# Performance work log

Hardware: AMD Instinct MI355X
Metric: run time of the kernel (lower is better)

## Reference

```python
import jax, jax.numpy as jnp
import numpy as np

D = 256      # embedding_dim
DI = 512     # inner dim = proj_factor * D
H = 4        # num heads
DH = DI // H # head dim
L = 4        # num blocks
K = 4        # causal conv kernel size

def _ln(x, g, b):
    mu = jnp.mean(x, -1, keepdims=True)
    v = jnp.var(x, -1, keepdims=True)
    return (x - mu) * jax.lax.rsqrt(v + 1e-5) * g + b

def _causal_conv(x, w, b):
    # x [B,S,DI], w [K,DI] depthwise causal conv
    S = x.shape[1]
    xp = jnp.pad(x, ((0, 0), (K - 1, 0), (0, 0)))
    out = b
    for j in range(K):
        out = out + xp[:, j:j + S, :] * w[j]
    return out

def _mlstm(q, k, v, ip, fp):
    # parallel stabilized mLSTM. q,k,v [B,S,H,DH]; ip,fp [B,S,H]
    q = q.transpose(0, 2, 1, 3)
    k = k.transpose(0, 2, 1, 3)
    v = v.transpose(0, 2, 1, 3)
    ip = ip.transpose(0, 2, 1)  # [B,H,S]
    fp = fp.transpose(0, 2, 1)
    lf = jax.nn.log_sigmoid(fp)                      # log forget gates
    Fc = jnp.cumsum(lf, axis=-1)
    Fc = jnp.concatenate([jnp.zeros_like(Fc[..., :1]), Fc], axis=-1)  # [B,H,S+1]
    logfg = Fc[..., 1:, None] - Fc[..., None, 1:]    # [B,H,S,S]: sum of log f over (s,t]
    S_len = q.shape[2]
    tri = jnp.tril(jnp.ones((S_len, S_len), dtype=bool))
    logD = jnp.where(tri, logfg + ip[..., None, :], jnp.float32(-1e30))
    m = jnp.max(logD, axis=-1, keepdims=True)        # stabilizer
    Dm = jnp.exp(logD - m)
    qk = jnp.einsum('bhtd,bhsd->bhts', q, k) * (DH ** -0.5)
    C = qk * Dm
    norm = jnp.maximum(jnp.abs(jnp.sum(C, axis=-1, keepdims=True)), jnp.exp(-m))
    h = jnp.einsum('bhts,bhsd->bhtd', C / (norm + 1e-6), v)
    return h.transpose(0, 2, 1, 3)

def _forward(x, time_features, Wp, bp, ln_g, ln_b, Wup, bup, conv_w, conv_b,
             Wq, Wk, Wv, Wif, bif, gn_g, gn_b, skip, Wdown, bdown,
             lnf_g, lnf_b, Wf, bf):
    B, S = x.shape
    xi = jnp.concatenate([x[..., None], time_features], axis=-1)  # [B,S,5]
    h = xi @ Wp + bp                                              # [B,S,D]
    for l in range(L):
        res = h
        hn = _ln(h, ln_g[l], ln_b[l])
        up = hn @ Wup[l] + bup[l]                 # [B,S,2*DI]
        xm, z = up[..., :DI], up[..., DI:]
        xc = jax.nn.silu(_causal_conv(xm, conv_w[l], conv_b[l]))
        q = (xc @ Wq[l]).reshape(B, S, H, DH)
        k = (xc @ Wk[l]).reshape(B, S, H, DH)
        v = (xm @ Wv[l]).reshape(B, S, H, DH)
        gi = jnp.concatenate([q.reshape(B, S, DI), k.reshape(B, S, DI), v.reshape(B, S, DI)], axis=-1)
        gates = gi @ Wif[l] + bif[l]              # [B,S,2H]
        ht = _mlstm(q, k, v, gates[..., :H], gates[..., H:])  # [B,S,H,DH]
        ht = _ln(ht, gn_g[l].reshape(H, DH), gn_b[l].reshape(H, DH)).reshape(B, S, DI)
        ht = ht + skip[l] * xc
        ht = ht * jax.nn.silu(z)
        h = res + ht @ Wdown[l] + bdown[l]
    h = _ln(h, lnf_g, lnf_b)
    return h[:, -1, :] @ Wf + bf                  # [B,1]

def setup_inputs():
    key = jax.random.key(0)
    ks = jax.random.split(key, 16)
    B, S = 8, 1024
    sd = jnp.float32(0.02)
    return {
        'x': jax.random.normal(ks[0], (B, S), jnp.float32),
        'time_features': jax.random.normal(ks[1], (B, S, 4), jnp.float32),
        'Wp': jax.random.normal(ks[2], (5, D)) * sd, 'bp': jnp.zeros((D,)),
        'ln_g': jnp.ones((L, D)), 'ln_b': jnp.zeros((L, D)),
        'Wup': jax.random.normal(ks[3], (L, D, 2 * DI)) * sd, 'bup': jnp.zeros((L, 2 * DI)),
        'conv_w': jax.random.normal(ks[4], (L, K, DI)) * sd, 'conv_b': jnp.zeros((L, DI)),
        'Wq': jax.random.normal(ks[5], (L, DI, DI)) * sd,
        'Wk': jax.random.normal(ks[6], (L, DI, DI)) * sd,
        'Wv': jax.random.normal(ks[7], (L, DI, DI)) * sd,
        'Wif': jax.random.normal(ks[8], (L, 3 * DI, 2 * H)) * sd, 'bif': jnp.zeros((L, 2 * H)),
        'gn_g': jnp.ones((L, DI)), 'gn_b': jnp.zeros((L, DI)),
        'skip': jnp.ones((L, DI)),
        'Wdown': jax.random.normal(ks[9], (L, DI, D)) * sd, 'bdown': jnp.zeros((L, D)),
        'lnf_g': jnp.ones((D,)), 'lnf_b': jnp.zeros((D,)),
        'Wf': jax.random.normal(ks[10], (D, 1)) * sd, 'bf': jnp.zeros((1,)),
    }

def reference(x, time_features, Wp, bp, ln_g, ln_b, Wup, bup, conv_w, conv_b,
              Wq, Wk, Wv, Wif, bif, gn_g, gn_b, skip, Wdown, bdown,
              lnf_g, lnf_b, Wf, bf):
    return _forward(x, time_features, Wp, bp, ln_g, ln_b, Wup, bup, conv_w, conv_b,
                    Wq, Wk, Wv, Wif, bif, gn_g, gn_b, skip, Wdown, bdown,
                    lnf_g, lnf_b, Wf, bf)
```

## Files before the change

### kernel.cpp

```cpp
#include <hip/hip_runtime.h>
#include <hip/hip_bf16.h>
#include <math.h>

#define S 1024
#define NLAYER 4

typedef __bf16 bf16x8 __attribute__((ext_vector_type(8)));
typedef float floatx4 __attribute__((ext_vector_type(4)));

__device__ __forceinline__ float wave_sum(float v) {
  #pragma unroll
  for (int off = 32; off > 0; off >>= 1) v += __shfl_xor(v, off, 64);
  return v;
}

__device__ __forceinline__ void wtrans_body(
    int bid, const float* Wup, const float* Wq, const float* Wk, const float* Wv,
    const float* Wdown, __bf16* WupT, __bf16* WqkT, __bf16* WvT, __bf16* WdownT) {
  __shared__ float T[32][33];
  int layer = bid / 1152, rr = bid % 1152;
  const float* src; __bf16* dst; int K, N, tile;
  if (rr < 256)       { src = Wup   + layer * 262144; dst = WupT  + layer * 262144;          K = 256; N = 1024; tile = rr; }
  else if (rr < 512)  { src = Wq    + layer * 262144; dst = WqkT  + layer * 524288;          K = 512; N = 512;  tile = rr - 256; }
  else if (rr < 768)  { src = Wk    + layer * 262144; dst = WqkT  + layer * 524288 + 262144; K = 512; N = 512;  tile = rr - 512; }
  else if (rr < 1024) { src = Wv    + layer * 262144; dst = WvT   + layer * 262144;          K = 512; N = 512;  tile = rr - 768; }
  else                { src = Wdown + layer * 131072; dst = WdownT + layer * 131072;         K = 512; N = 256;  tile = rr - 1024; }
  int ntn = N >> 5;
  int tk = tile / ntn, tn = tile % ntn;
  int tid = threadIdx.x;
  int r = tid >> 3, c4 = (tid & 7) * 4;
  float4 v = *(const float4*)(src + (size_t)(tk * 32 + r) * N + tn * 32 + c4);
  T[c4 + 0][r] = v.x; T[c4 + 1][r] = v.y; T[c4 + 2][r] = v.z; T[c4 + 3][r] = v.w;
  __syncthreads();
  __bf16 o[4];
  #pragma unroll
  for (int j = 0; j < 4; ++j) o[j] = (__bf16)T[r][c4 + j];
  *(uint2*)(dst + (size_t)(tn * 32 + r) * K + tk * 32 + c4) = *(uint2*)o;
}

__device__ __forceinline__ void wgprep_body(
    int bid, const float* Wq, const float* Wk, const float* Wv,
    const float* Wif, float* wg) {
  int l = bid >> 8;
  int rem = bid & 255;
  int sel = rem >> 7;
  int kg = rem & 127;
  int tid = threadIdx.x;
  int wv = tid >> 6, lane = tid & 63;
  int k = kg * 4 + wv;
  const float* wif = Wif + (size_t)l * 1536 * 8;
  float part[8] = {0, 0, 0, 0, 0, 0, 0, 0};
  if (sel == 0) {
    const float* qr = Wq + (size_t)l * 262144 + (size_t)k * 512;
    const float* kr = Wk + (size_t)l * 262144 + (size_t)k * 512;
    #pragma unroll
    for (int i = 0; i < 8; ++i) {
      int n = lane + i * 64;
      float qv = qr[n], kv = kr[n];
      const float* wq8 = wif + (size_t)n * 8;
      const float* wk8 = wif + (size_t)(512 + n) * 8;
      #pragma unroll
      for (int j = 0; j < 8; ++j) part[j] += qv * wq8[j] + kv * wk8[j];
    }
  } else {
    const float* vr = Wv + (size_t)l * 262144 + (size_t)k * 512;
    #pragma unroll
    for (int i = 0; i < 8; ++i) {
      int n = lane + i * 64;
      float vv = vr[n];
      const float* wv8 = wif + (size_t)(1024 + n) * 8;
      #pragma unroll
      for (int j = 0; j < 8; ++j) part[j] += vv * wv8[j];
    }
  }
  #pragma unroll
  for (int j = 0; j < 8; ++j) part[j] = wave_sum(part[j]);
  if (lane < 8) wg[(size_t)l * 8192 + sel * 4096 + (size_t)k * 8 + lane] = part[lane];
}

__device__ __forceinline__ void embed_body(
    int row, const float* x, const float* tf, const float* Wp, const float* bp,
    const float* g, const float* b, float* h, __bf16* hn) {
  int n = threadIdx.x;
  float xv = x[row];
  const float* t4 = tf + (size_t)row * 4;
  float acc = bp[n] + xv * Wp[n];
  acc += t4[0] * Wp[256 + n];
  acc += t4[1] * Wp[512 + n];
  acc += t4[2] * Wp[768 + n];
  acc += t4[3] * Wp[1024 + n];
  h[(size_t)row * 256 + n] = acc;
  __shared__ float red[4];
  int wid = n >> 6, lane = n & 63;
  float s = wave_sum(acc);
  if (lane == 0) red[wid] = s;
  __syncthreads();
  float mu = (red[0] + red[1] + red[2] + red[3]) * (1.f / 256.f);
  __syncthreads();
  float d = acc - mu;
  float s2 = wave_sum(d * d);
  if (lane == 0) red[wid] = s2;
  __syncthreads();
  float var = (red[0] + red[1] + red[2] + red[3]) * (1.f / 256.f);
  float rs = rsqrtf(var + 1e-5f);
  hn[(size_t)row * 256 + n] = (__bf16)(d * rs * g[n] + b[n]);
}

__global__ __launch_bounds__(256) void prep_kernel(
    const float* __restrict__ x, const float* __restrict__ tf,
    const float* __restrict__ Wp, const float* __restrict__ bp,
    const float* __restrict__ ln_g, const float* __restrict__ ln_b,
    const float* __restrict__ Wup, const float* __restrict__ Wq,
    const float* __restrict__ Wk, const float* __restrict__ Wv,
    const float* __restrict__ Wdown, const float* __restrict__ Wif,
    __bf16* __restrict__ WupT, __bf16* __restrict__ WqkT,
    __bf16* __restrict__ WvT, __bf16* __restrict__ WdownT,
    float* __restrict__ wg, float* __restrict__ h, __bf16* __restrict__ hn) {
  int bid = blockIdx.x;
  if (bid < 4608) {
    wtrans_body(bid, Wup, Wq, Wk, Wv, Wdown, WupT, WqkT, WvT, WdownT);
  } else if (bid < 4608 + 1024) {
    wgprep_body(bid - 4608, Wq, Wk, Wv, Wif, wg);
  } else {
    embed_body(bid - 5632, x, tf, Wp, bp, ln_g, ln_b, h, hn);
  }
}

template <int TM, int MODE, int ACC>
__device__ __forceinline__ void hgemm_body(
    char* smem_raw,
    const __bf16* __restrict__ A, int lda,
    const __bf16* __restrict__ BT, int Kdim,
    const float* __restrict__ bias,
    void* __restrict__ Cout, int ldc, int bxi, int byi) {
  auto As = (__bf16(*)[40])smem_raw;
  auto Bs = (__bf16(*)[40])(smem_raw + (size_t)TM * 160);
  int tid = threadIdx.x;
  int bm = bxi * TM, bn = byi * 128;
  int wid = tid >> 6, lane = tid & 63;
  int wr = wid >> 1, wc = wid & 1;
  int lg = lane >> 4, li = lane & 15;
  constexpr int MI = TM / 32;
  constexpr int WROW = TM / 2;
  floatx4 acc[MI][4];
  #pragma unroll
  for (int i = 0; i < MI; ++i)
    #pragma unroll
    for (int j = 0; j < 4; ++j) acc[i][j] = (floatx4)(0.f);

  int arow = tid >> 2, aseg = tid & 3;
  bf16x8 pa0, pa1, pb0, pb1;
  auto pre = [&](int k0) {
    pa0 = *(const bf16x8*)(A + (size_t)(bm + arow) * lda + k0 + aseg * 8);
    if constexpr (TM == 128)
      pa1 = *(const bf16x8*)(A + (size_t)(bm + arow + 64) * lda + k0 + aseg * 8);
    pb0 = *(const bf16x8*)(BT + (size_t)(bn + arow) * Kdim + k0 + aseg * 8);
    pb1 = *(const bf16x8*)(BT + (size_t)(bn + arow + 64) * Kdim + k0 + aseg * 8);
  };
  auto stor = [&](int buf) {
    *(bf16x8*)&As[buf * TM + arow][aseg * 8] = pa0;
    if constexpr (TM == 128) *(bf16x8*)&As[buf * TM + arow + 64][aseg * 8] = pa1;
    *(bf16x8*)&Bs[buf * 128 + arow][aseg * 8] = pb0;
    *(bf16x8*)&Bs[buf * 128 + arow + 64][aseg * 8] = pb1;
  };
  pre(0);
  stor(0);
  if (32 < Kdim) pre(32);
  int cur = 0;
  for (int k0 = 0; k0 < Kdim; k0 += 32) {
    __syncthreads();
    bf16x8 af[MI], bfr[4];
    #pragma unroll
    for (int mi = 0; mi < MI; ++mi)
      af[mi] = *(const bf16x8*)&As[cur * TM + wr * WROW + mi * 16 + li][lg * 8];
    #pragma unroll
    for (int ni = 0; ni < 4; ++ni)
      bfr[ni] = *(const bf16x8*)&Bs[cur * 128 + wc * 64 + ni * 16 + li][lg * 8];
    #pragma unroll
    for (int mi = 0; mi < MI; ++mi)
      #pragma unroll
      for (int ni = 0; ni < 4; ++ni)
        acc[mi][ni] = __builtin_amdgcn_mfma_f32_16x16x32_bf16(af[mi], bfr[ni], acc[mi][ni], 0, 0, 0);
    if (k0 + 32 < Kdim) {
      stor(cur ^ 1);
      if (k0 + 64 < Kdim) pre(k0 + 64);
    }
    cur ^= 1;
  }
  if constexpr (MODE == 1) {
    __bf16* eb = (__bf16*)smem_raw;
    const int PITCH = 136;
    __bf16* C = (__bf16*)Cout;
    #pragma unroll
    for (int mi = 0; mi < MI; ++mi) {
      __syncthreads();
      #pragma unroll
      for (int ni = 0; ni < 4; ++ni) {
        int col = wc * 64 + ni * 16 + li;
        float bz = bias ? bias[bn + col] : 0.f;
        #pragma unroll
        for (int r = 0; r < 4; ++r) {
          int lr = wr * 16 + lg * 4 + r;
          eb[lr * PITCH + col] = (__bf16)(acc[mi][ni][r] + bz);
        }
      }
      __syncthreads();
      #pragma unroll
      for (int i = 0; i < 2; ++i) {
        int lr = (tid >> 4) + i * 16;
        int c8 = (tid & 15) * 8;
        bf16x8 v = *(const bf16x8*)&eb[lr * PITCH + c8];
        int row_g = bm + (lr >> 4) * 64 + mi * 16 + (lr & 15);
        *(bf16x8*)(C + (size_t)row_g * ldc + bn + c8) = v;
      }
    }
  } else {
    #pragma unroll
    for (int mi = 0; mi < MI; ++mi) {
      int row = bm + wr * WROW + mi * 16 + lg * 4;
      #pragma unroll
      for (int ni = 0; ni < 4; ++ni) {
        int col = bn + wc * 64 + ni * 16 + li;
        if constexpr (MODE == 2) {
          __bf16 o4[4];
          #pragma unroll
          for (int r = 0; r < 4; ++r) o4[r] = (__bf16)acc[mi][ni][r];
          __bf16* vt = (__bf16*)Cout;
          size_t off = ((size_t)((row >> 10) * 4 + (col >> 7)) * 128 + (col & 127)) * 1024 + (row & 1023);
          *(uint2*)(vt + off) = *(uint2*)o4;
        } else {
          float bz = bias ? bias[col] : 0.f;
          float* C = (float*)Cout;
          #pragma unroll
          for (int r = 0; r < 4; ++r) {
            float v = acc[mi][ni][r] + bz;
            if (ACC) v += C[(size_t)(row + r) * ldc + col];
            C[(size_t)(row + r) * ldc + col] = v;
          }
        }
      }
    }
  }
}

template <int TM, int MODE, int ACC>
__global__ __launch_bounds__(256) void hgemm(
    const __bf16* __restrict__ A, int lda,
    const __bf16* __restrict__ BT, int Kdim,
    const float* __restrict__ bias,
    void* __restrict__ Cout, int ldc) {
  extern __shared__ char smem[];
  hgemm_body<TM, MODE, ACC>(smem, A, lda, BT, Kdim, bias, Cout, ldc,
                            blockIdx.x, blockIdx.y);
}

__device__ __forceinline__ void scan_body(
    int bh, int lane, const float* __restrict__ gates, float* __restrict__ gout,
    float* __restrict__ Mout, float* __restrict__ NFout) {
  int bb = bh >> 2, hh = bh & 3;
  float ip[16], pf[16];
  #pragma unroll
  for (int i = 0; i < 16; ++i) {
    int t = lane * 16 + i;
    const float* grow = gates + ((size_t)(bb * S + t)) * 8;
    ip[i] = grow[hh];
    float fp = grow[4 + hh];
    float lf = fminf(fp, 0.f) - log1pf(__expf(-fabsf(fp)));
    pf[i] = (i == 0) ? lf : pf[i - 1] + lf;
  }
  float T = pf[15];
  float inc = T;
  #pragma unroll
  for (int off = 1; off < 64; off <<= 1) {
    float v = __shfl_up(inc, off, 64);
    if (lane >= off) inc += v;
  }
  float excl = inc - T;
  float F[16], g[16], pm[16];
  #pragma unroll
  for (int i = 0; i < 16; ++i) {
    F[i] = excl + pf[i];
    g[i] = ip[i] - F[i];
    pm[i] = (i == 0) ? g[0] : fmaxf(pm[i - 1], g[i]);
  }
  float Mx = pm[15];
  float incm = Mx;
  #pragma unroll
  for (int off = 1; off < 64; off <<= 1) {
    float v = __shfl_up(incm, off, 64);
    if (lane >= off) incm = fmaxf(incm, v);
  }
  float em = __shfl_up(incm, 1, 64);
  if (lane == 0) em = -3.4e38f;
  #pragma unroll
  for (int i = 0; i < 16; ++i) {
    int t = lane * 16 + i;
    size_t o = (size_t)bh * S + t;
    float M = fmaxf(em, pm[i]);
    gout[o] = g[i];
    Mout[o] = M;
    NFout[o] = __expf(-F[i] - M);
  }
}

__global__ __launch_bounds__(256) void qkv_kernel(
    const __bf16* __restrict__ xc, const __bf16* __restrict__ WqkT,
    __bf16* __restrict__ qk, const __bf16* __restrict__ up,
    const __bf16* __restrict__ WvT, __bf16* __restrict__ vT,
    const float* __restrict__ gates, float* __restrict__ gbuf,
    float* __restrict__ Mbuf, float* __restrict__ NFbuf) {
  extern __shared__ char smem[];
  if (blockIdx.y < 8) {
    hgemm_body<128, 1, 0>(smem, xc, 512, WqkT, 512, nullptr, qk, 1024,
                          blockIdx.x, blockIdx.y);
  } else if (blockIdx.y < 16) {
    int j = blockIdx.y - 8;
    hgemm_body<64, 2, 0>(smem, up, 1024, WvT, 512, nullptr, vT, 0,
                         blockIdx.x * 2 + (j & 1), j >> 1);
  } else {
    if (blockIdx.x < 32 && threadIdx.x < 64)
      scan_body(blockIdx.x, threadIdx.x, gates, gbuf, Mbuf, NFbuf);
  }
}

__global__ __launch_bounds__(256) void dgemm_ln_kernel(
    const __bf16* __restrict__ A, const __bf16* __restrict__ BT,
    const float* __restrict__ bias, float* __restrict__ h,
    const float* __restrict__ lng, const float* __restrict__ lnb,
    __bf16* __restrict__ hn,
    const float* __restrict__ lnfg, const float* __restrict__ lnfb,
    const float* __restrict__ Wf, const float* __restrict__ bf,
    float* __restrict__ out) {
  __shared__ __bf16 As[2 * 32][40];
  __shared__ __bf16 Bs[2 * 256][40];
  __shared__ float redS[2][32], redQ[2][32];
  int tid = threadIdx.x;
  int bm = blockIdx.x * 32;
  int wid = tid >> 6, lane = tid & 63;
  int wr = wid >> 1, wc = wid & 1;
  int lg = lane >> 4, li = lane & 15;
  floatx4 acc[8];
  #pragma unroll
  for (int j = 0; j < 8; ++j) acc[j] = (floatx4)(0.f);

  int arow = tid >> 2, aseg = tid & 3;
  bf16x8 pa, pb[4];
  auto pre = [&](int k0) {
    if (tid < 128)
      pa = *(const bf16x8*)(A + (size_t)(bm + arow) * 512 + k0 + aseg * 8);
    #pragma unroll
    for (int i = 0; i < 4; ++i)
      pb[i] = *(const bf16x8*)(BT + (size_t)(arow + i * 64) * 512 + k0 + aseg * 8);
  };
  auto stor = [&](int buf) {
    if (tid < 128) *(bf16x8*)&As[buf * 32 + arow][aseg * 8] = pa;
    #pragma unroll
    for (int i = 0; i < 4; ++i)
      *(bf16x8*)&Bs[buf * 256 + arow + i * 64][aseg * 8] = pb[i];
  };
  pre(0);
  stor(0);
  pre(32);
  int cur = 0;
  for (int k0 = 0; k0 < 512; k0 += 32) {
    __syncthreads();
    bf16x8 af = *(const bf16x8*)&As[cur * 32 + wr * 16 + li][lg * 8];
    #pragma unroll
    for (int ni = 0; ni < 8; ++ni) {
      bf16x8 bfr = *(const bf16x8*)&Bs[cur * 256 + wc * 128 + ni * 16 + li][lg * 8];
      acc[ni] = __builtin_amdgcn_mfma_f32_16x16x32_bf16(af, bfr, acc[ni], 0, 0, 0);
    }
    if (k0 + 32 < 512) {
      stor(cur ^ 1);
      if (k0 + 64 < 512) pre(k0 + 64);
    }
    cur ^= 1;
  }
  #pragma unroll
  for (int r = 0; r < 4; ++r) {
    int lr = wr * 16 + lg * 4 + r;
    int row = bm + lr;
    float s1 = 0.f, s2 = 0.f;
    #pragma unroll
    for (int ni = 0; ni < 8; ++ni) {
      int col = wc * 128 + ni * 16 + li;
      float v = acc[ni][r] + bias[col] + h[(size_t)row * 256 + col];
      acc[ni][r] = v;
      h[(size_t)row * 256 + col] = v;
      s1 += v;
      s2 += v * v;
    }
    s1 += __shfl_xor(s1, 1, 64); s1 += __shfl_xor(s1, 2, 64);
    s1 += __shfl_xor(s1, 4, 64); s1 += __shfl_xor(s1, 8, 64);
    s2 += __shfl_xor(s2, 1, 64); s2 += __shfl_xor(s2, 2, 64);
    s2 += __shfl_xor(s2, 4, 64); s2 += __shfl_xor(s2, 8, 64);
    if (li == 0) { redS[wc][lr] = s1; redQ[wc][lr] = s2; }
  }
  __syncthreads();
  if (lng) {
    #pragma unroll
    for (int r = 0; r < 4; ++r) {
      int lr = wr * 16 + lg * 4 + r;
      int row = bm + lr;
      float s1 = redS[0][lr] + redS[1][lr];
      float s2 = redQ[0][lr] + redQ[1][lr];
      float mu = s1 * (1.f / 256.f);
      float var = s2 * (1.f / 256.f) - mu * mu;
      float rs = rsqrtf(var + 1e-5f);
      #pragma unroll
      for (int ni = 0; ni < 8; ++ni) {
        int col = wc * 128 + ni * 16 + li;
        hn[(size_t)row * 256 + col] = (__bf16)((acc[ni][r] - mu) * rs * lng[col] + lnb[col]);
      }
    }
  } else if ((bm & 1023) == 992) {
    if (wr == 1 && lg == 3) {
      float s1 = redS[0][31] + redS[1][31];
      float s2 = redQ[0][31] + redQ[1][31];
      float mu = s1 * (1.f / 256.f);
      float var = s2 * (1.f / 256.f) - mu * mu;
      float rs = rsqrtf(var + 1e-5f);
      float p = 0.f;
      #pragma unroll
      for (int ni = 0; ni < 8; ++ni) {
        int col = wc * 128 + ni * 16 + li;
        float ln = (acc[ni][3] - mu) * rs * lnfg[col] + lnfb[col];
        p += ln * Wf[col];
      }
      p += __shfl_xor(p, 1, 64); p += __shfl_xor(p, 2, 64);
      p += __shfl_xor(p, 4, 64); p += __shfl_xor(p, 8, 64);
      if (li == 0) redS[wc][0] = p;
    }
    __syncthreads();
    if (tid == 0) out[bm >> 10] = redS[0][0] + redS[1][0] + bf[0];
  }
}

__global__ __launch_bounds__(256) void conv_silu_kernel(
    const __bf16* __restrict__ up, const float* __restrict__ cw,
    const float* __restrict__ cb, const float* __restrict__ wg,
    const float* __restrict__ bif, __bf16* __restrict__ xc,
    float* __restrict__ gates) {
  int tid = threadIdx.x;
  int wv = tid >> 6, lane = tid & 63;
  int row = blockIdx.x * 4 + wv;
  int c8 = lane * 8;
  int t = row & (S - 1);
  float acc[8];
  *(float4*)&acc[0] = *(const float4*)(cb + c8);
  *(float4*)&acc[4] = *(const float4*)(cb + c8 + 4);
  float xm[8];
  #pragma unroll
  for (int j = 0; j < 4; ++j) {
    int tt = t - 3 + j;
    if (tt >= 0) {
      bf16x8 xv = *(const bf16x8*)(up + (size_t)(row - 3 + j) * 1024 + c8);
      float4 w0 = *(const float4*)(cw + j * 512 + c8);
      float4 w1 = *(const float4*)(cw + j * 512 + c8 + 4);
      acc[0] += w0.x * (float)xv[0]; acc[1] += w0.y * (float)xv[1];
      acc[2] += w0.z * (float)xv[2]; acc[3] += w0.w * (float)xv[3];
      acc[4] += w1.x * (float)xv[4]; acc[5] += w1.y * (float)xv[5];
      acc[6] += w1.z * (float)xv[6]; acc[7] += w1.w * (float)xv[7];
      if (j == 3) {
        #pragma unroll
        for (int m = 0; m < 8; ++m) xm[m] = (float)xv[m];
      }
    }
  }
  bf16x8 o;
  float xcs[8];
  #pragma unroll
  for (int m = 0; m < 8; ++m) {
    float sg = 1.f / (1.f + __expf(-acc[m]));
    xcs[m] = acc[m] * sg;
    o[m] = (__bf16)xcs[m];
  }
  *(bf16x8*)(xc + (size_t)row * 512 + c8) = o;
  const float* w1 = wg + (size_t)c8 * 8;
  const float* w2 = wg + 4096 + (size_t)c8 * 8;
  float part[8] = {0, 0, 0, 0, 0, 0, 0, 0};
  #pragma unroll
  for (int m = 0; m < 8; ++m) {
    const float* a = w1 + m * 8;
    const float* b = w2 + m * 8;
    #pragma unroll
    for (int j = 0; j < 8; ++j) part[j] += xcs[m] * a[j] + xm[m] * b[j];
  }
  #pragma unroll
  for (int j = 0; j < 8; ++j) part[j] = wave_sum(part[j]);
  if (lane < 8) gates[(size_t)row * 8 + lane] = part[lane] + bif[lane];
}

__global__ __launch_bounds__(512, 1) void attn_kernel(
    const __bf16* __restrict__ qk, const __bf16* __restrict__ vT,
    const float* __restrict__ gbuf, const float* __restrict__ Mbuf,
    const float* __restrict__ NFbuf,
    const float* __restrict__ gn_g, const float* __restrict__ gn_b,
    const float* __restrict__ skip,
    const __bf16* __restrict__ xc, const __bf16* __restrict__ up,
    __bf16* __restrict__ hd) {
  __shared__ __bf16 Ks[64][136];
  __shared__ __bf16 Vs[128][72];
  __shared__ __bf16 plds[8][16][72];
  __shared__ float gls[64];
  __shared__ float glds[128], blds[128], slds[128];
  int px = blockIdx.y, bh = blockIdx.x;
  int tqA = px, tqB = 15 - px;
  int bb = bh >> 2, hh = bh & 3;
  int tid = threadIdx.x;
  int wv = tid >> 6, lane = tid & 63;
  int sel = wv >> 2, wl = wv & 3;
  int lg = lane >> 4, li = lane & 15;
  int tq = (sel == 0) ? tqA : tqB;
  int tb = tq * 64 + wl * 16;
  const float scale = 0.08838834764831845f;

  if (tid < 128) {
    glds[tid] = gn_g[hh * 128 + tid];
    blds[tid] = gn_b[hh * 128 + tid];
    slds[tid] = skip[hh * 128 + tid];
  }

  bf16x8 aq[4];
  {
    const __bf16* qp = qk + ((size_t)(bb * S + tb + li)) * 1024 + hh * 128 + lg * 8;
    #pragma unroll
    for (int cd = 0; cd < 4; ++cd) aq[cd] = *(const bf16x8*)(qp + cd * 32);
  }
  float ml[4], nf[4];
  #pragma unroll
  for (int r = 0; r < 4; ++r) {
    ml[r] = Mbuf[(size_t)bh * S + tb + lg * 4 + r];
    nf[r] = NFbuf[(size_t)bh * S + tb + lg * 4 + r];
  }

  floatx4 oacc[8];
  #pragma unroll
  for (int df = 0; df < 8; ++df) oacc[df] = (floatx4)(0.f);
  float rs[4] = {0, 0, 0, 0};

  int krow = tid >> 3, kcol = tid & 7;
  bf16x8 kreg0, kreg1, vreg0, vreg1;
  float greg = 0.f;
  auto preload = [&](int st) {
    int s0 = st * 64;
    const __bf16* kp = qk + ((size_t)(bb * S + s0 + krow)) * 1024 + 512 + hh * 128;
    kreg0 = *(const bf16x8*)(kp + kcol * 8);
    kreg1 = *(const bf16x8*)(kp + 64 + kcol * 8);
    vreg0 = *(const bf16x8*)(vT + ((size_t)(bh * 128 + krow)) * 1024 + s0 + kcol * 8);
    vreg1 = *(const bf16x8*)(vT + ((size_t)(bh * 128 + 64 + krow)) * 1024 + s0 + kcol * 8);
    if (tid < 64) greg = gbuf[(size_t)bh * S + s0 + tid];
  };
  preload(0);

  for (int st = 0; st <= tqB; ++st) {
    __syncthreads();
    *(bf16x8*)&Ks[krow][kcol * 8] = kreg0;
    *(bf16x8*)&Ks[krow][64 + kcol * 8] = kreg1;
    *(bf16x8*)&Vs[krow][kcol * 8] = vreg0;
    *(bf16x8*)&Vs[64 + krow][kcol * 8] = vreg1;
    if (tid < 64) gls[tid] = greg;
    __syncthreads();
    if (st < tqB) preload(st + 1);

    if (st <= tq) {
      int s0 = st * 64;
      #pragma unroll
      for (int ns = 0; ns < 4; ++ns) {
        bf16x8 bk0 = *(const bf16x8*)&Ks[ns * 16 + li][lg * 8];
        bf16x8 bk1 = *(const bf16x8*)&Ks[ns * 16 + li][32 + lg * 8];
        bf16x8 bk2 = *(const bf16x8*)&Ks[ns * 16 + li][64 + lg * 8];
        bf16x8 bk3 = *(const bf16x8*)&Ks[ns * 16 + li][96 + lg * 8];
        int s = s0 + ns * 16 + li;
        float gv = gls[ns * 16 + li];
        floatx4 pa = (floatx4)(0.f);
        pa = __builtin_amdgcn_mfma_f32_16x16x32_bf16(aq[0], bk0, pa, 0, 0, 0);
        pa = __builtin_amdgcn_mfma_f32_16x16x32_bf16(aq[1], bk1, pa, 0, 0, 0);
        pa = __builtin_amdgcn_mfma_f32_16x16x32_bf16(aq[2], bk2, pa, 0, 0, 0);
        pa = __builtin_amdgcn_mfma_f32_16x16x32_bf16(aq[3], bk3, pa, 0, 0, 0);
        #pragma unroll
        for (int r = 0; r < 4; ++r) {
          int t = tb + lg * 4 + r;
          float val = pa[r] * scale * __expf(gv - ml[r]);
          float w = (s <= t) ? val : 0.f;
          rs[r] += w;
          plds[wv][lg * 4 + r][ns * 16 + li] = (__bf16)w;
        }
      }
      bf16x8 ap0 = *(const bf16x8*)&plds[wv][li][lg * 8];
      bf16x8 ap1 = *(const bf16x8*)&plds[wv][li][32 + lg * 8];
      #pragma unroll
      for (int df = 0; df < 8; ++df) {
        bf16x8 bv0 = *(const bf16x8*)&Vs[df * 16 + li][lg * 8];
        bf16x8 bv1 = *(const bf16x8*)&Vs[df * 16 + li][32 + lg * 8];
        oacc[df] = __builtin_amdgcn_mfma_f32_16x16x32_bf16(ap0, bv0, oacc[df], 0, 0, 0);
        oacc[df] = __builtin_amdgcn_mfma_f32_16x16x32_bf16(ap1, bv1, oacc[df], 0, 0, 0);
      }
    }
  }
  #pragma unroll
  for (int r = 0; r < 4; ++r) {
    float a = rs[r];
    a += __shfl_xor(a, 1, 64); a += __shfl_xor(a, 2, 64);
    a += __shfl_xor(a, 4, 64); a += __shfl_xor(a, 8, 64);
    rs[r] = a;
  }
  #pragma unroll
  for (int r = 0; r < 4; ++r) {
    float inv = 1.f / (fmaxf(fabsf(rs[r]), nf[r]) + 1e-6f);
    float v8[8], s1 = 0.f, s2 = 0.f;
    #pragma unroll
    for (int df = 0; df < 8; ++df) {
      float v = oacc[df][r] * inv;
      v8[df] = v;
      s1 += v;
      s2 += v * v;
    }
    s1 += __shfl_xor(s1, 1, 64); s1 += __shfl_xor(s1, 2, 64);
    s1 += __shfl_xor(s1, 4, 64); s1 += __shfl_xor(s1, 8, 64);
    s2 += __shfl_xor(s2, 1, 64); s2 += __shfl_xor(s2, 2, 64);
    s2 += __shfl_xor(s2, 4, 64); s2 += __shfl_xor(s2, 8, 64);
    float mu = s1 * (1.f / 128.f);
    float var = s2 * (1.f / 128.f) - mu * mu;
    float rq = rsqrtf(var + 1e-5f);
    int t = tb + lg * 4 + r;
    const __bf16* xr = xc + ((size_t)(bb * S + t)) * 512 + hh * 128 + li;
    const __bf16* zr = up + ((size_t)(bb * S + t)) * 1024 + 512 + hh * 128 + li;
    __bf16* od = hd + ((size_t)(bb * S + t)) * 512 + hh * 128 + li;
    #pragma unroll
    for (int df = 0; df < 8; ++df) {
      int c = df * 16 + li;
      float ln = (v8[df] - mu) * rq * glds[c] + blds[c];
      float val = ln + slds[c] * (float)xr[df * 16];
      float z = (float)zr[df * 16];
      float sg = 1.f / (1.f + __expf(-z));
      od[df * 16] = (__bf16)(val * (z * sg));
    }
  }
}

extern "C" void kernel_launch(void* const* d_in, const int* in_sizes, int n_in,
                              void* d_out, int out_size, void* d_ws, size_t ws_size,
                              hipStream_t stream) {
  const float* x      = (const float*)d_in[0];
  const float* tf     = (const float*)d_in[1];
  const float* Wp     = (const float*)d_in[2];
  const float* bp     = (const float*)d_in[3];
  const float* ln_g   = (const float*)d_in[4];
  const float* ln_b   = (const float*)d_in[5];
  const float* Wup    = (const float*)d_in[6];
  const float* bup    = (const float*)d_in[7];
  const float* conv_w = (const float*)d_in[8];
  const float* conv_b = (const float*)d_in[9];
  const float* Wq     = (const float*)d_in[10];
  const float* Wk     = (const float*)d_in[11];
  const float* Wv     = (const float*)d_in[12];
  const float* Wif    = (const float*)d_in[13];
  const float* bif    = (const float*)d_in[14];
  const float* gn_g   = (const float*)d_in[15];
  const float* gn_b   = (const float*)d_in[16];
  const float* skip   = (const float*)d_in[17];
  const float* Wdown  = (const float*)d_in[18];
  const float* bdown  = (const float*)d_in[19];
  const float* lnf_g  = (const float*)d_in[20];
  const float* lnf_b  = (const float*)d_in[21];
  const float* Wf     = (const float*)d_in[22];
  const float* bf     = (const float*)d_in[23];
  float* out = (float*)d_out;

  float* h     = (float*)d_ws;
  float* gates = h + 2097152;
  float* gbuf  = gates + 65536;
  float* Mbuf  = gbuf + 32768;
  float* NFbuf = Mbuf + 32768;
  float* wgbuf = NFbuf + 32768;
  __bf16* hn   = (__bf16*)(wgbuf + 32768);
  __bf16* up   = hn + 2097152;
  __bf16* xc   = up + 8388608;
  __bf16* qk   = xc + 4194304;
  __bf16* vT   = qk + 8388608;
  __bf16* hd   = vT + 4194304;
  __bf16* WupT   = hd + 4194304;
  __bf16* WqkT   = WupT + 1048576;
  __bf16* WvT    = WqkT + 2097152;
  __bf16* WdownT = WvT + 1048576;

  prep_kernel<<<13824, 256, 0, stream>>>(
      x, tf, Wp, bp, ln_g, ln_b, Wup, Wq, Wk, Wv, Wdown, Wif,
      WupT, WqkT, WvT, WdownT, wgbuf, h, hn);
  for (int l = 0; l < NLAYER; ++l) {
    hgemm<128, 1, 0><<<dim3(64, 8), 256, 40960, stream>>>(
        hn, 256, WupT + (size_t)l * 262144, 256, bup + l * 1024, up, 1024);
    conv_silu_kernel<<<2048, 256, 0, stream>>>(up, conv_w + l * 2048, conv_b + l * 512,
                                               wgbuf + l * 8192, bif + l * 8, xc, gates);
    qkv_kernel<<<dim3(64, 17), 256, 40960, stream>>>(
        xc, WqkT + (size_t)l * 524288, qk, up, WvT + (size_t)l * 262144, vT,
        gates, gbuf, Mbuf, NFbuf);
    attn_kernel<<<dim3(32, 8), 512, 0, stream>>>(
        qk, vT, gbuf, Mbuf, NFbuf, gn_g + l * 512, gn_b + l * 512, skip + l * 512,
        xc, up, hd);
    const float* lng = (l + 1 < NLAYER) ? (ln_g + (l + 1) * 256) : nullptr;
    const float* lnb = (l + 1 < NLAYER) ? (ln_b + (l + 1) * 256) : nullptr;
    dgemm_ln_kernel<<<256, 256, 0, stream>>>(
        hd, WdownT + (size_t)l * 131072, bdown + l * 256, h, lng, lnb, hn,
        lnf_g, lnf_b, Wf, bf, out);
  }
}
```

Measured before the change: 593.9 us.

## Split paired-query-tile attention blocks into one 256-thread block per query tile

After: 588.8 us. About the same (-0.9%).

```diff
diff --git a/kernel.cpp b/kernel.cpp
--- a/kernel.cpp
+++ b/kernel.cpp
@@ -491,7 +491,7 @@
   if (lane < 8) gates[(size_t)row * 8 + lane] = part[lane] + bif[lane];
 }
 
-__global__ __launch_bounds__(512, 1) void attn_kernel(
+__global__ __launch_bounds__(256, 1) void attn_kernel(
     const __bf16* __restrict__ qk, const __bf16* __restrict__ vT,
     const float* __restrict__ gbuf, const float* __restrict__ Mbuf,
     const float* __restrict__ NFbuf,
@@ -501,18 +501,16 @@
     __bf16* __restrict__ hd) {
   __shared__ __bf16 Ks[64][136];
   __shared__ __bf16 Vs[128][72];
-  __shared__ __bf16 plds[8][16][72];
+  __shared__ __bf16 plds[4][16][72];
   __shared__ float gls[64];
   __shared__ float glds[128], blds[128], slds[128];
-  int px = blockIdx.y, bh = blockIdx.x;
-  int tqA = px, tqB = 15 - px;
+  int bh = blockIdx.x;
+  int tq = 15 - blockIdx.y;
   int bb = bh >> 2, hh = bh & 3;
   int tid = threadIdx.x;
   int wv = tid >> 6, lane = tid & 63;
-  int sel = wv >> 2, wl = wv & 3;
   int lg = lane >> 4, li = lane & 15;
-  int tq = (sel == 0) ? tqA : tqB;
-  int tb = tq * 64 + wl * 16;
+  int tb = tq * 64 + wv * 16;
   const float scale = 0.08838834764831845f;
 
   if (tid < 128) {
@@ -540,62 +538,65 @@
   float rs[4] = {0, 0, 0, 0};
 
   int krow = tid >> 3, kcol = tid & 7;
-  bf16x8 kreg0, kreg1, vreg0, vreg1;
+  bf16x8 kreg[4], vreg[4];
   float greg = 0.f;
   auto preload = [&](int st) {
     int s0 = st * 64;
     const __bf16* kp = qk + ((size_t)(bb * S + s0 + krow)) * 1024 + 512 + hh * 128;
-    kreg0 = *(const bf16x8*)(kp + kcol * 8);
-    kreg1 = *(const bf16x8*)(kp + 64 + kcol * 8);
-    vreg0 = *(const bf16x8*)(vT + ((size_t)(bh * 128 + krow)) * 1024 + s0 + kcol * 8);
-    vreg1 = *(const bf16x8*)(vT + ((size_t)(bh * 128 + 64 + krow)) * 1024 + s0 + kcol * 8);
+    kreg[0] = *(const bf16x8*)(kp + kcol * 8);
+    kreg[1] = *(const bf16x8*)(kp + (size_t)32 * 1024 + kcol * 8);
+    kreg[2] = *(const bf16x8*)(kp + 64 + kcol * 8);
+    kreg[3] = *(const bf16x8*)(kp + (size_t)32 * 1024 + 64 + kcol * 8);
+    #pragma unroll
+    for (int i = 0; i < 4; ++i)
+      vreg[i] = *(const bf16x8*)(vT + ((size_t)(bh * 128 + krow + i * 32)) * 1024 + s0 + kcol * 8);
     if (tid < 64) greg = gbuf[(size_t)bh * S + s0 + tid];
   };
   preload(0);
 
-  for (int st = 0; st <= tqB; ++st) {
+  for (int st = 0; st <= tq; ++st) {
     __syncthreads();
-    *(bf16x8*)&Ks[krow][kcol * 8] = kreg0;
-    *(bf16x8*)&Ks[krow][64 + kcol * 8] = kreg1;
-    *(bf16x8*)&Vs[krow][kcol * 8] = vreg0;
-    *(bf16x8*)&Vs[64 + krow][kcol * 8] = vreg1;
+    *(bf16x8*)&Ks[krow][kcol * 8] = kreg[0];
+    *(bf16x8*)&Ks[krow + 32][kcol * 8] = kreg[1];
+    *(bf16x8*)&Ks[krow][64 + kcol * 8] = kreg[2];
+    *(bf16x8*)&Ks[krow + 32][64 + kcol * 8] = kreg[3];
+    #pragma unroll
+    for (int i = 0; i < 4; ++i) *(bf16x8*)&Vs[krow + i * 32][kcol * 8] = vreg[i];
     if (tid < 64) gls[tid] = greg;
     __syncthreads();
-    if (st < tqB) preload(st + 1);
-
-    if (st <= tq) {
-      int s0 = st * 64;
-      #pragma unroll
-      for (int ns = 0; ns < 4; ++ns) {
-        bf16x8 bk0 = *(const bf16x8*)&Ks[ns * 16 + li][lg * 8];
-        bf16x8 bk1 = *(const bf16x8*)&Ks[ns * 16 + li][32 + lg * 8];
-        bf16x8 bk2 = *(const bf16x8*)&Ks[ns * 16 + li][64 + lg * 8];
-        bf16x8 bk3 = *(const bf16x8*)&Ks[ns * 16 + li][96 + lg * 8];
-        int s = s0 + ns * 16 + li;
-        float gv = gls[ns * 16 + li];
-        floatx4 pa = (floatx4)(0.f);
-        pa = __builtin_amdgcn_mfma_f32_16x16x32_bf16(aq[0], bk0, pa, 0, 0, 0);
-        pa = __builtin_amdgcn_mfma_f32_16x16x32_bf16(aq[1], bk1, pa, 0, 0, 0);
-        pa = __builtin_amdgcn_mfma_f32_16x16x32_bf16(aq[2], bk2, pa, 0, 0, 0);
-        pa = __builtin_amdgcn_mfma_f32_16x16x32_bf16(aq[3], bk3, pa, 0, 0, 0);
-        #pragma unroll
-        for (int r = 0; r < 4; ++r) {
-          int t = tb + lg * 4 + r;
-          float val = pa[r] * scale * __expf(gv - ml[r]);
-          float w = (s <= t) ? val : 0.f;
-          rs[r] += w;
-          plds[wv][lg * 4 + r][ns * 16 + li] = (__bf16)w;
-        }
+    if (st < tq) preload(st + 1);
+
+    int s0 = st * 64;
+    #pragma unroll
+    for (int ns = 0; ns < 4; ++ns) {
+      bf16x8 bk0 = *(const bf16x8*)&Ks[ns * 16 + li][lg * 8];
+      bf16x8 bk1 = *(const bf16x8*)&Ks[ns * 16 + li][32 + lg * 8];
+      bf16x8 bk2 = *(const bf16x8*)&Ks[ns * 16 + li][64 + lg * 8];
+      bf16x8 bk3 = *(const bf16x8*)&Ks[ns * 16 + li][96 + lg * 8];
+      int s = s0 + ns * 16 + li;
+      float gv = gls[ns * 16 + li];
+      floatx4 pa = (floatx4)(0.f);
+      pa = __builtin_amdgcn_mfma_f32_16x16x32_bf16(aq[0], bk0, pa, 0, 0, 0);
+      pa = __builtin_amdgcn_mfma_f32_16x16x32_bf16(aq[1], bk1, pa, 0, 0, 0);
+      pa = __builtin_amdgcn_mfma_f32_16x16x32_bf16(aq[2], bk2, pa, 0, 0, 0);
+      pa = __builtin_amdgcn_mfma_f32_16x16x32_bf16(aq[3], bk3, pa, 0, 0, 0);
+      #pragma unroll
+      for (int r = 0; r < 4; ++r) {
+        int t = tb + lg * 4 + r;
+        float val = pa[r] * scale * __expf(gv - ml[r]);
+        float w = (s <= t) ? val : 0.f;
+        rs[r] += w;
+        plds[wv][lg * 4 + r][ns * 16 + li] = (__bf16)w;
       }
-      bf16x8 ap0 = *(const bf16x8*)&plds[wv][li][lg * 8];
-      bf16x8 ap1 = *(const bf16x8*)&plds[wv][li][32 + lg * 8];
-      #pragma unroll
-      for (int df = 0; df < 8; ++df) {
-        bf16x8 bv0 = *(const bf16x8*)&Vs[df * 16 + li][lg * 8];
-        bf16x8 bv1 = *(const bf16x8*)&Vs[df * 16 + li][32 + lg * 8];
-        oacc[df] = __builtin_amdgcn_mfma_f32_16x16x32_bf16(ap0, bv0, oacc[df], 0, 0, 0);
-        oacc[df] = __builtin_amdgcn_mfma_f32_16x16x32_bf16(ap1, bv1, oacc[df], 0, 0, 0);
-      }
+    }
+    bf16x8 ap0 = *(const bf16x8*)&plds[wv][li][lg * 8];
+    bf16x8 ap1 = *(const bf16x8*)&plds[wv][li][32 + lg * 8];
+    #pragma unroll
+    for (int df = 0; df < 8; ++df) {
+      bf16x8 bv0 = *(const bf16x8*)&Vs[df * 16 + li][lg * 8];
+      bf16x8 bv1 = *(const bf16x8*)&Vs[df * 16 + li][32 + lg * 8];
+      oacc[df] = __builtin_amdgcn_mfma_f32_16x16x32_bf16(ap0, bv0, oacc[df], 0, 0, 0);
+      oacc[df] = __builtin_amdgcn_mfma_f32_16x16x32_bf16(ap1, bv1, oacc[df], 0, 0, 0);
     }
   }
   #pragma unroll
@@ -696,7 +697,7 @@
     qkv_kernel<<<dim3(64, 17), 256, 40960, stream>>>(
         xc, WqkT + (size_t)l * 524288, qk, up, WvT + (size_t)l * 262144, vT,
         gates, gbuf, Mbuf, NFbuf);
-    attn_kernel<<<dim3(32, 8), 512, 0, stream>>>(
+    attn_kernel<<<dim3(32, 16), 256, 0, stream>>>(
         qk, vT, gbuf, Mbuf, NFbuf, gn_g + l * 512, gn_b + l * 512, skip + l * 512,
         xc, up, hd);
     const float* lng = (l + 1 < NLAYER) ? (ln_g + (l + 1) * 256) : nullptr;
```
